# Performance work log

Hardware: AMD Instinct MI355X
Metric: run time of the kernel (lower is better)

Reference implementation:

```python
import jax, jax.numpy as jnp
import numpy as np

B, T, L, H, I, W_OUT = 64, 512, 2, 512, 128, 32


def setup_inputs() -> dict:
    key = jax.random.key(0)
    ks = jax.random.split(key, 12)
    stdv = 1.0 / np.sqrt(H)
    u = lambda k, shape: jax.random.uniform(k, shape, jnp.float32, -stdv, stdv)
    return {
        "x": jax.random.normal(ks[0], (B, T, I), jnp.float32),
        "noise": jax.random.normal(ks[1], (B, T, L, H), jnp.float32) * 0.1,
        "W_ih0": u(ks[2], (H, I)),
        "W_ih1": u(ks[3], (H, H)),
        "W_hh0": u(ks[4], (H, H)),
        "W_hh1": u(ks[5], (H, H)),
        "b_ih0": u(ks[6], (H,)),
        "b_ih1": u(ks[7], (H,)),
        "b_hh0": u(ks[8], (H,)),
        "b_hh1": u(ks[9], (H,)),
        "fc_w": u(ks[10], (W_OUT, H)),
        "fc_b": u(ks[11], (W_OUT,)),
    }


def reference(x, noise, W_ih0, W_ih1, W_hh0, W_hh1, b_ih0, b_ih1, b_hh0, b_hh1, fc_w, fc_b):
    # Sequential two-layer tanh RNN; scan over time keeps hidden state resident.
    h0 = jnp.zeros((B, H), x.dtype)
    h1 = jnp.zeros((B, H), x.dtype)

    def step(carry, inp):
        h0, h1 = carry
        x_t, n_t = inp  # x_t: [B,I], n_t: [B,L,H]
        h0 = jnp.tanh(x_t @ W_ih0.T + b_ih0 + h0 @ W_hh0.T + b_hh0 + n_t[:, 0, :])
        h1 = jnp.tanh(h0 @ W_ih1.T + b_ih1 + h1 @ W_hh1.T + b_hh1 + n_t[:, 1, :])
        return (h0, h1), None

    # time-major scan inputs
    (h0, h1), _ = jax.lax.scan(step, (h0, h1), (jnp.swapaxes(x, 0, 1), jnp.swapaxes(noise, 0, 1)))
    return h1 @ fc_w.T + fc_b  # [B, wheel_len]
```

## Files before the change

kernel.cpp:

```cpp
#include <hip/hip_runtime.h>


#define T_STEPS 512
#define NBATCH  64
#define DRING   32
#define THR_LEAD 20

typedef _Float16 half2v __attribute__((ext_vector_type(2)));
typedef _Float16 f16x8  __attribute__((ext_vector_type(8)));
typedef float    f32x4  __attribute__((ext_vector_type(4)));

__device__ __forceinline__ unsigned pack2(float a, float b) {
    _Float16 fa = (_Float16)a, fb = (_Float16)b;
    unsigned short ua = __builtin_bit_cast(unsigned short, fa);
    unsigned short ub = __builtin_bit_cast(unsigned short, fb);
    return (unsigned)ua | ((unsigned)ub << 16);
}

__device__ __forceinline__ float fast_tanh(float xv) {
    float e2 = __builtin_amdgcn_exp2f(xv * 2.885390082f);
    return 1.f - 2.f * __builtin_amdgcn_rcpf(e2 + 1.f);
}

__device__ __forceinline__ f32x4 mfma16(uint4 a, uint4 b, f32x4 c) {
    return __builtin_amdgcn_mfma_f32_16x16x32_f16(
        __builtin_bit_cast(f16x8, a), __builtin_bit_cast(f16x8, b), c, 0, 0, 0);
}

__device__ __forceinline__ void bar_lgkm() {
    asm volatile("s_waitcnt lgkmcnt(0)\n\ts_barrier" ::: "memory");
}

__device__ __forceinline__ float ntload_f(const float* p) {
    return __builtin_nontemporal_load(p);
}
__device__ __forceinline__ float2 ntload_f2(const float* p) {
    float a = __builtin_nontemporal_load(p);
    float b = __builtin_nontemporal_load(p + 1);
    return make_float2(a, b);
}

__device__ __forceinline__ unsigned poll1(unsigned long long* p, unsigned tag,
                                          long& budget) {
    unsigned long long v = __hip_atomic_load(p, __ATOMIC_RELAXED, __HIP_MEMORY_SCOPE_AGENT);
    while ((unsigned)(v >> 32) != tag && budget > 0) {
        v = __hip_atomic_load(p, __ATOMIC_RELAXED, __HIP_MEMORY_SCOPE_AGENT);
        --budget;
    }
    return (unsigned)v;
}

__device__ __forceinline__ unsigned poll_sent(unsigned long long* p,
                                              unsigned long long* sent,
                                              unsigned tag, long& budget) {
    unsigned long long sv = __hip_atomic_load(sent, __ATOMIC_RELAXED, __HIP_MEMORY_SCOPE_AGENT);
    while ((unsigned)(sv >> 32) != tag && budget > 0) {
        __builtin_amdgcn_s_sleep(1);
        sv = __hip_atomic_load(sent, __ATOMIC_RELAXED, __HIP_MEMORY_SCOPE_AGENT);
        --budget;
    }
    return poll1(p, tag, budget);
}

#define NWPF (4 * 16 * 16 * 64)

__global__ void init_pack(const float* __restrict__ Wih0, const float* __restrict__ Whh0,
                          const float* __restrict__ Wih1, const float* __restrict__ Whh1,
                          uint4* __restrict__ wp0, uint4* __restrict__ wp1,
                          int* __restrict__ prog) {
    int gid = blockIdx.x * 256 + threadIdx.x;
    if (gid == 32) prog[32] = prog[32] + 1;
    if (gid < 32) prog[gid] = 0;
    if (gid < NWPF) {
        int lane = gid & 63, f = (gid >> 6) & 15, w = (gid >> 10) & 15, s = gid >> 14;
        uint4 o = make_uint4(0, 0, 0, 0);
        if (w < 10) {
            int rt = f >> 1, ktl = f & 1;
            int r = s * 128 + rt * 16 + (lane & 15);
            unsigned dv[4];
#pragma unroll
            for (int d = 0; d < 4; ++d) {
                int kp = 32 * w + ktl * 16 + ((lane >> 4) * 4) + d;
                float w0, w1;
                if (kp < 64) { w0 = Wih0[r * 128 + 2 * kp]; w1 = Wih0[r * 128 + 2 * kp + 1]; }
                else { int p0 = kp - 64;
                       w0 = Whh0[r * 512 + 2 * p0]; w1 = Whh0[r * 512 + 2 * p0 + 1]; }
                dv[d] = pack2(w0, w1);
            }
            o = make_uint4(dv[0], dv[1], dv[2], dv[3]);
        }
        wp0[gid] = o;
    } else if (gid < 2 * NWPF) {
        int idx = gid - NWPF;
        int lane = idx & 63, f = (idx >> 6) & 15, w = (idx >> 10) & 15, s = idx >> 14;
        int rt = f >> 1, ktl = f & 1;
        int r = s * 128 + rt * 16 + (lane & 15);
        unsigned dv[4];
#pragma unroll
        for (int d = 0; d < 4; ++d) {
            int kp = 32 * w + ktl * 16 + ((lane >> 4) * 4) + d;
            float w0, w1;
            if (kp < 256) { w0 = Wih1[r * 512 + 2 * kp]; w1 = Wih1[r * 512 + 2 * kp + 1]; }
            else { int p1 = kp - 256;
                   w0 = Whh1[r * 512 + 2 * p1]; w1 = Whh1[r * 512 + 2 * p1 + 1]; }
            dv[d] = pack2(w0, w1);
        }
        wp1[idx] = make_uint4(dv[0], dv[1], dv[2], dv[3]);
    }
}

template <int LAYER>
__device__ __forceinline__ void run_layer(
    int b0, int s, int L, int pair,
    const float* __restrict__ x, const float* __restrict__ noise,
    const uint4* __restrict__ wp,
    const float* __restrict__ bih, const float* __restrict__ bhh,
    unsigned long long* __restrict__ hb0, unsigned long long* __restrict__ hb1,
    int* __restrict__ prog,
    const float* __restrict__ fcw, const float* __restrict__ fcb,
    float* __restrict__ out) {
    constexpr int NP = (LAYER == 0) ? 10 : 16;

    const int w = L >> 6, lane = L & 63;
    const int j31 = lane & 31, bbl = lane >> 5;
    const unsigned tagbase = ((unsigned)prog[32]) << 10;
    long budget = 2000000000L;

    const bool active   = (LAYER == 1) || (w < 10);
    const bool isX      = (LAYER == 0) && (w < 2);
    const bool isPF     = (LAYER == 1) && (w < 8);
    const bool isOwn    = (LAYER == 0) ? (w == 2 + 2 * s || w == 3 + 2 * s)
                                       : (w == 8 + 2 * s || w == 9 + 2 * s);
    const bool isRemote = active && !isX && !isPF && !isOwn;

    uint4 wfr[16];
#pragma unroll
    for (int f = 0; f < 16; ++f) {
        wfr[f] = wp[(size_t)(((s * 16 + w) * 16) + f) * 64 + lane];
        asm volatile("" : "+v"(wfr[f].x), "+v"(wfr[f].y), "+v"(wfr[f].z), "+v"(wfr[f].w));
    }

    __shared__ __align__(16) unsigned strip[16][64];
    __shared__ __align__(16) float psum[NP][2][128];
    for (int i = L; i < 16 * 64; i += 1024) ((unsigned*)strip)[i] = 0u;

    const bool isRed = (L < 256);
    const int bbr = L >> 7, rw = L & 127;
    const int rgl = s * 128 + rw;
    float cb = 0.f, nz = 0.f;
    if (isRed) {
        cb = bih[rgl] + bhh[rgl];
        nz = ntload_f(&noise[(((size_t)(b0 + bbr) * T_STEPS + 0) * 2 + LAYER) * 512 + rgl]);
    }
    __syncthreads();

    unsigned long long pf = 0;
    float2 xf = make_float2(0.f, 0.f);
    if constexpr (LAYER == 1) {
        if (isPF) {
            unsigned long long* base = &hb0[((size_t)0 * NBATCH + (b0 + bbl)) * 256];
            unsigned v = poll_sent(base + (32 * w + j31), base + (32 * w + 31),
                                   tagbase + 1, budget);
            pf = ((unsigned long long)(tagbase + 1) << 32) | v;
        }
    } else {
        if (isX)
            xf = ntload_f2(x + ((size_t)(b0 + bbl) * T_STEPS + 0) * 128 + 2 * (32 * w + j31));
    }

    int known = 0;
    const int colm = lane & 15, kg = lane >> 4;

    for (int t = 0; t < T_STEPS; ++t) {
        const bool last = (t == T_STEPS - 1);
        __builtin_amdgcn_s_setprio(1);

        if constexpr (LAYER == 1) {
            if (isPF) {
                unsigned want = tagbase + (unsigned)t + 1;
                if ((unsigned)(pf >> 32) != want) {
                    __builtin_amdgcn_s_setprio(0);
                    unsigned long long* base =
                        &hb0[((size_t)(t & (DRING - 1)) * NBATCH + (b0 + bbl)) * 256];
                    unsigned v = poll_sent(base + (32 * w + j31), base + (32 * w + 31),
                                           want, budget);
                    pf = ((unsigned long long)want << 32) | v;
                    __builtin_amdgcn_s_setprio(1);
                }
                strip[w][bbl * 32 + j31] = (unsigned)pf;
                if (!last)
                    pf = __hip_atomic_load(&hb0[((size_t)((t + 1) & (DRING - 1)) * NBATCH +
                                                 (b0 + bbl)) * 256 + (32 * w + j31)],
                                           __ATOMIC_RELAXED, __HIP_MEMORY_SCOPE_AGENT);
            } else if (isRemote) {
                if (t > 0) {
                    unsigned long long* base =
                        &hb1[((size_t)((t - 1) & 3) * NBATCH + (b0 + bbl)) * 256];
                    __builtin_amdgcn_s_setprio(0);
                    unsigned v = poll_sent(base + (32 * (w - 8) + j31),
                                           base + (32 * (w - 8) + 31),
                                           tagbase + (unsigned)t, budget);
                    __builtin_amdgcn_s_setprio(1);
                    strip[w][bbl * 32 + j31] = v;
                }
            }
        } else {
            if (isX) {
                strip[w][bbl * 32 + j31] = pack2(xf.x, xf.y);
                if (!last)
                    xf = ntload_f2(x + ((size_t)(b0 + bbl) * T_STEPS + (t + 1)) * 128 +
                                   2 * (32 * w + j31));
            } else if (isRemote) {
                if (t > 0) {
                    unsigned long long* base =
                        &hb0[((size_t)((t - 1) & (DRING - 1)) * NBATCH + (b0 + bbl)) * 256];
                    __builtin_amdgcn_s_setprio(0);
                    unsigned v = poll_sent(base + (32 * w - 64 + j31),
                                           base + (32 * w - 64 + 31),
                                           tagbase + (unsigned)t, budget);
                    __builtin_amdgcn_s_setprio(1);
                    strip[w][bbl * 32 + j31] = v;
                }
            }
        }

        float nznext = 0.f;
        if (!last && isRed)
            nznext = ntload_f(&noise[(((size_t)(b0 + bbr) * T_STEPS + (t + 1)) * 2 + LAYER) * 512 + rgl]);

        if (active) {
            const unsigned* sb = &strip[w][(colm & 1) * 32 + kg * 4];
            uint4 B0 = *(const uint4*)&sb[0];
            uint4 B1 = *(const uint4*)&sb[16];
#pragma unroll
            for (int rt = 0; rt < 8; ++rt) {
                f32x4 C = {0.f, 0.f, 0.f, 0.f};
                C = mfma16(wfr[2 * rt + 0], B0, C);
                C = mfma16(wfr[2 * rt + 1], B1, C);
                if (colm < 2)
                    *(f32x4*)&psum[w][colm][rt * 16 + 4 * kg] = C;
            }
        }

        bar_lgkm();

        if (isRed) {
            float sum = 0.f;
#pragma unroll
            for (int g = 0; g < NP; ++g) sum += psum[g][bbr][rw];
            float h = fast_tanh(sum + cb + nz);
            float hnb = __shfl_down(h, 1);
            if ((L & 1) == 0) {
                unsigned pv = pack2(h, hnb);
                int pr = s * 64 + (rw >> 1);
                unsigned long long atom =
                    ((unsigned long long)(tagbase + (unsigned)t + 1) << 32) |
                    (unsigned long long)pv;
                if constexpr (LAYER == 0) {
                    if (t - known > THR_LEAD) {
                        __builtin_amdgcn_s_setprio(0);
                        while (t - known > THR_LEAD && budget > 0) {
                            __builtin_amdgcn_s_sleep(2);
                            known = __hip_atomic_load(&prog[pair], __ATOMIC_RELAXED,
                                                      __HIP_MEMORY_SCOPE_AGENT);
                            --budget;
                        }
                        __builtin_amdgcn_s_setprio(1);
                    }
                    __hip_atomic_store(&hb0[((size_t)(t & (DRING - 1)) * NBATCH + (b0 + bbr)) * 256 + pr],
                                       atom, __ATOMIC_RELAXED, __HIP_MEMORY_SCOPE_AGENT);
                    strip[2 + (pr >> 5)][bbr * 32 + (pr & 31)] = pv;
                } else {
                    __hip_atomic_store(&hb1[((size_t)(t & 3) * NBATCH + (b0 + bbr)) * 256 + pr],
                                       atom, __ATOMIC_RELAXED, __HIP_MEMORY_SCOPE_AGENT);
                    strip[8 + (pr >> 5)][bbr * 32 + (pr & 31)] = pv;
                }
            }
            nz = nznext;
        }
        if constexpr (LAYER == 1) {
            if (s == 0 && L == 960 && t > 1)
                __hip_atomic_store(&prog[pair], t - 2, __ATOMIC_RELAXED,
                                   __HIP_MEMORY_SCOPE_AGENT);
        }
        bar_lgkm();
        __builtin_amdgcn_s_setprio(0);
    }

    if constexpr (LAYER == 1) {
        if (s == 0) {
            __shared__ float hs[2][512];
            __shared__ float part[2][512];
            if (L < 512) {
                int bl = L >> 8, pr = L & 255;
                unsigned v = poll1(&hb1[((size_t)((T_STEPS - 1) & 3) * NBATCH + (b0 + bl)) * 256 + pr],
                                   tagbase + (unsigned)T_STEPS, budget);
                half2v h2 = __builtin_bit_cast(half2v, v);
                hs[bl][2 * pr] = (float)h2.x; hs[bl][2 * pr + 1] = (float)h2.y;
            }
            __syncthreads();
            {
                int bl = L >> 9, rest = L & 511, o = rest & 31, seg = rest >> 5;
                const float* wr = fcw + o * 512 + seg * 32;
                const float* hr = &hs[bl][seg * 32];
                float a = 0.f;
#pragma unroll
                for (int k = 0; k < 32; ++k) a = fmaf(wr[k], hr[k], a);
                part[bl][rest] = a;
            }
            __syncthreads();
            if (L < 64) {
                int bl = L >> 5, o = L & 31;
                float ssum = fcb[o];
#pragma unroll
                for (int sgi = 0; sgi < 16; ++sgi) ssum += part[bl][sgi * 32 + o];
                out[(b0 + bl) * 32 + o] = ssum;
            }
        }
    }
}

__global__ __launch_bounds__(1024, 4)
void rnn_dual(const float* __restrict__ x, const float* __restrict__ noise,
              const uint4* __restrict__ wp0, const uint4* __restrict__ wp1,
              const float* __restrict__ bih0, const float* __restrict__ bhh0,
              const float* __restrict__ bih1, const float* __restrict__ bhh1,
              const float* __restrict__ fcw, const float* __restrict__ fcb,
              unsigned long long* __restrict__ hb0,
              unsigned long long* __restrict__ hb1,
              int* __restrict__ prog,
              float* __restrict__ out) {
    const int L = threadIdx.x;
    const int gid = blockIdx.x;
    const int cl = gid & 63;
    const int s = gid >> 6;
    const int layer = cl >> 5;
    const int pair = cl & 31;
    const int b0 = pair * 2;
    if (layer == 0)
        run_layer<0>(b0, s, L, pair, x, noise, wp0, bih0, bhh0,
                     hb0, hb1, prog, nullptr, nullptr, nullptr);
    else
        run_layer<1>(b0, s, L, pair, x, noise, wp1, bih1, bhh1,
                     hb0, hb1, prog, fcw, fcb, out);
}

extern "C" void kernel_launch(void* const* d_in, const int* in_sizes, int n_in,
                              void* d_out, int out_size, void* d_ws, size_t ws_size,
                              hipStream_t stream) {
    const float* x     = (const float*)d_in[0];
    const float* noise = (const float*)d_in[1];
    const float* Wih0  = (const float*)d_in[2];
    const float* Wih1  = (const float*)d_in[3];
    const float* Whh0  = (const float*)d_in[4];
    const float* Whh1  = (const float*)d_in[5];
    const float* bih0  = (const float*)d_in[6];
    const float* bih1  = (const float*)d_in[7];
    const float* bhh0  = (const float*)d_in[8];
    const float* bhh1  = (const float*)d_in[9];
    const float* fcw   = (const float*)d_in[10];
    const float* fcb   = (const float*)d_in[11];
    float* out = (float*)d_out;

    char* ws = (char*)d_ws;
    size_t o = 0;
    uint4* wp0 = (uint4*)(ws + o); o += (size_t)NWPF * 16;
    uint4* wp1 = (uint4*)(ws + o); o += (size_t)NWPF * 16;
    unsigned long long* hb0 = (unsigned long long*)(ws + o);
    o += (size_t)DRING * NBATCH * 256 * 8;
    unsigned long long* hb1 = (unsigned long long*)(ws + o);
    o += (size_t)4 * NBATCH * 256 * 8;
    int* prog = (int*)(ws + o); o += 33 * sizeof(int);

    const int total = 2 * NWPF;
    init_pack<<<(total + 255) / 256, 256, 0, stream>>>(Wih0, Whh0, Wih1, Whh1,
                                                       wp0, wp1, prog);
    rnn_dual<<<256, 1024, 0, stream>>>(x, noise, wp0, wp1, bih0, bhh0, bih1, bhh1,
                                       fcw, fcb, hb0, hb1, prog, out);
}
```

Baseline: 1.075 ms.

## Double-buffer partial sums, drop end-of-step barrier, poll own slice via global

Result: slower. 1.155 ms (+7.5%).

```diff
diff --git a/kernel.cpp b/kernel.cpp
--- a/kernel.cpp
+++ b/kernel.cpp
@@ -50,15 +50,18 @@
     return (unsigned)v;
 }
 
-__device__ __forceinline__ unsigned poll_sent(unsigned long long* p,
+__device__ __forceinline__ unsigned poll_spec(unsigned long long* p,
                                               unsigned long long* sent,
                                               unsigned tag, long& budget) {
+    unsigned long long v  = __hip_atomic_load(p,    __ATOMIC_RELAXED, __HIP_MEMORY_SCOPE_AGENT);
     unsigned long long sv = __hip_atomic_load(sent, __ATOMIC_RELAXED, __HIP_MEMORY_SCOPE_AGENT);
     while ((unsigned)(sv >> 32) != tag && budget > 0) {
         __builtin_amdgcn_s_sleep(1);
+        v  = __hip_atomic_load(p,    __ATOMIC_RELAXED, __HIP_MEMORY_SCOPE_AGENT);
         sv = __hip_atomic_load(sent, __ATOMIC_RELAXED, __HIP_MEMORY_SCOPE_AGENT);
         --budget;
     }
+    if ((unsigned)(v >> 32) == tag) return (unsigned)v;
     return poll1(p, tag, budget);
 }
 
@@ -126,12 +129,10 @@
     const unsigned tagbase = ((unsigned)prog[32]) << 10;
     long budget = 2000000000L;
 
-    const bool active   = (LAYER == 1) || (w < 10);
-    const bool isX      = (LAYER == 0) && (w < 2);
-    const bool isPF     = (LAYER == 1) && (w < 8);
-    const bool isOwn    = (LAYER == 0) ? (w == 2 + 2 * s || w == 3 + 2 * s)
-                                       : (w == 8 + 2 * s || w == 9 + 2 * s);
-    const bool isRemote = active && !isX && !isPF && !isOwn;
+    const bool active = (LAYER == 1) || (w < 10);
+    const bool isX    = (LAYER == 0) && (w < 2);
+    const bool isPF   = (LAYER == 1) && (w < 8);
+    const bool isPoll = (LAYER == 0) ? (w >= 2 && w < 10) : (w >= 8);
 
     uint4 wfr[16];
 #pragma unroll
@@ -141,11 +142,12 @@
     }
 
     __shared__ __align__(16) unsigned strip[16][64];
-    __shared__ __align__(16) float psum[NP][2][128];
+    __shared__ __align__(16) float psum[2][NP][2][128];
     for (int i = L; i < 16 * 64; i += 1024) ((unsigned*)strip)[i] = 0u;
 
-    const bool isRed = (L < 256);
-    const int bbr = L >> 7, rw = L & 127;
+    const bool isRed = (LAYER == 0) ? (L >= 640 && L < 896) : (L < 256);
+    const int ur  = (LAYER == 0) ? (L - 640) : L;
+    const int bbr = (ur >> 7) & 1, rw = ur & 127;
     const int rgl = s * 128 + rw;
     float cb = 0.f, nz = 0.f;
     if (isRed) {
@@ -158,9 +160,8 @@
     float2 xf = make_float2(0.f, 0.f);
     if constexpr (LAYER == 1) {
         if (isPF) {
-            unsigned long long* base = &hb0[((size_t)0 * NBATCH + (b0 + bbl)) * 256];
-            unsigned v = poll_sent(base + (32 * w + j31), base + (32 * w + 31),
-                                   tagbase + 1, budget);
+            unsigned long long* sb = &hb0[((size_t)0 * NBATCH + (b0 + bbl)) * 256 + 32 * w];
+            unsigned v = poll_spec(sb + j31, sb + 31, tagbase + 1, budget);
             pf = ((unsigned long long)(tagbase + 1) << 32) | v;
         }
     } else {
@@ -172,6 +173,7 @@
     const int colm = lane & 15, kg = lane >> 4;
 
     for (int t = 0; t < T_STEPS; ++t) {
+        const int p = t & 1;
         const bool last = (t == T_STEPS - 1);
         __builtin_amdgcn_s_setprio(1);
 
@@ -180,10 +182,9 @@
                 unsigned want = tagbase + (unsigned)t + 1;
                 if ((unsigned)(pf >> 32) != want) {
                     __builtin_amdgcn_s_setprio(0);
-                    unsigned long long* base =
-                        &hb0[((size_t)(t & (DRING - 1)) * NBATCH + (b0 + bbl)) * 256];
-                    unsigned v = poll_sent(base + (32 * w + j31), base + (32 * w + 31),
-                                           want, budget);
+                    unsigned long long* sb =
+                        &hb0[((size_t)(t & (DRING - 1)) * NBATCH + (b0 + bbl)) * 256 + 32 * w];
+                    unsigned v = poll_spec(sb + j31, sb + 31, want, budget);
                     pf = ((unsigned long long)want << 32) | v;
                     __builtin_amdgcn_s_setprio(1);
                 }
@@ -192,14 +193,12 @@
                     pf = __hip_atomic_load(&hb0[((size_t)((t + 1) & (DRING - 1)) * NBATCH +
                                                  (b0 + bbl)) * 256 + (32 * w + j31)],
                                            __ATOMIC_RELAXED, __HIP_MEMORY_SCOPE_AGENT);
-            } else if (isRemote) {
+            } else {
                 if (t > 0) {
-                    unsigned long long* base =
-                        &hb1[((size_t)((t - 1) & 3) * NBATCH + (b0 + bbl)) * 256];
+                    unsigned long long* sb =
+                        &hb1[((size_t)((t - 1) & 3) * NBATCH + (b0 + bbl)) * 256 + 32 * (w - 8)];
                     __builtin_amdgcn_s_setprio(0);
-                    unsigned v = poll_sent(base + (32 * (w - 8) + j31),
-                                           base + (32 * (w - 8) + 31),
-                                           tagbase + (unsigned)t, budget);
+                    unsigned v = poll_spec(sb + j31, sb + 31, tagbase + (unsigned)t, budget);
                     __builtin_amdgcn_s_setprio(1);
                     strip[w][bbl * 32 + j31] = v;
                 }
@@ -210,14 +209,13 @@
                 if (!last)
                     xf = ntload_f2(x + ((size_t)(b0 + bbl) * T_STEPS + (t + 1)) * 128 +
                                    2 * (32 * w + j31));
-            } else if (isRemote) {
+            } else if (isPoll) {
                 if (t > 0) {
-                    unsigned long long* base =
-                        &hb0[((size_t)((t - 1) & (DRING - 1)) * NBATCH + (b0 + bbl)) * 256];
+                    unsigned long long* sb =
+                        &hb0[((size_t)((t - 1) & (DRING - 1)) * NBATCH + (b0 + bbl)) * 256 +
+                             (32 * w - 64)];
                     __builtin_amdgcn_s_setprio(0);
-                    unsigned v = poll_sent(base + (32 * w - 64 + j31),
-                                           base + (32 * w - 64 + 31),
-                                           tagbase + (unsigned)t, budget);
+                    unsigned v = poll_spec(sb + j31, sb + 31, tagbase + (unsigned)t, budget);
                     __builtin_amdgcn_s_setprio(1);
                     strip[w][bbl * 32 + j31] = v;
                 }
@@ -238,7 +236,7 @@
                 C = mfma16(wfr[2 * rt + 0], B0, C);
                 C = mfma16(wfr[2 * rt + 1], B1, C);
                 if (colm < 2)
-                    *(f32x4*)&psum[w][colm][rt * 16 + 4 * kg] = C;
+                    *(f32x4*)&psum[p][w][colm][rt * 16 + 4 * kg] = C;
             }
         }
 
@@ -247,10 +245,10 @@
         if (isRed) {
             float sum = 0.f;
 #pragma unroll
-            for (int g = 0; g < NP; ++g) sum += psum[g][bbr][rw];
+            for (int g = 0; g < NP; ++g) sum += psum[p][g][bbr][rw];
             float h = fast_tanh(sum + cb + nz);
             float hnb = __shfl_down(h, 1);
-            if ((L & 1) == 0) {
+            if ((ur & 1) == 0) {
                 unsigned pv = pack2(h, hnb);
                 int pr = s * 64 + (rw >> 1);
                 unsigned long long atom =
@@ -269,11 +267,9 @@
                     }
                     __hip_atomic_store(&hb0[((size_t)(t & (DRING - 1)) * NBATCH + (b0 + bbr)) * 256 + pr],
                                        atom, __ATOMIC_RELAXED, __HIP_MEMORY_SCOPE_AGENT);
-                    strip[2 + (pr >> 5)][bbr * 32 + (pr & 31)] = pv;
                 } else {
                     __hip_atomic_store(&hb1[((size_t)(t & 3) * NBATCH + (b0 + bbr)) * 256 + pr],
                                        atom, __ATOMIC_RELAXED, __HIP_MEMORY_SCOPE_AGENT);
-                    strip[8 + (pr >> 5)][bbr * 32 + (pr & 31)] = pv;
                 }
             }
             nz = nznext;
@@ -283,37 +279,38 @@
                 __hip_atomic_store(&prog[pair], t - 2, __ATOMIC_RELAXED,
                                    __HIP_MEMORY_SCOPE_AGENT);
         }
-        bar_lgkm();
         __builtin_amdgcn_s_setprio(0);
     }
 
     if constexpr (LAYER == 1) {
         if (s == 0) {
-            __shared__ float hs[2][512];
-            __shared__ float part[2][512];
+            __syncthreads();
+            float* hsbuf = (float*)&psum[0][0][0][0];
+            float* partb = hsbuf + 1024;
             if (L < 512) {
                 int bl = L >> 8, pr = L & 255;
                 unsigned v = poll1(&hb1[((size_t)((T_STEPS - 1) & 3) * NBATCH + (b0 + bl)) * 256 + pr],
                                    tagbase + (unsigned)T_STEPS, budget);
                 half2v h2 = __builtin_bit_cast(half2v, v);
-                hs[bl][2 * pr] = (float)h2.x; hs[bl][2 * pr + 1] = (float)h2.y;
+                hsbuf[bl * 512 + 2 * pr] = (float)h2.x;
+                hsbuf[bl * 512 + 2 * pr + 1] = (float)h2.y;
             }
             __syncthreads();
             {
                 int bl = L >> 9, rest = L & 511, o = rest & 31, seg = rest >> 5;
                 const float* wr = fcw + o * 512 + seg * 32;
-                const float* hr = &hs[bl][seg * 32];
+                const float* hr = &hsbuf[bl * 512 + seg * 32];
                 float a = 0.f;
 #pragma unroll
                 for (int k = 0; k < 32; ++k) a = fmaf(wr[k], hr[k], a);
-                part[bl][rest] = a;
+                partb[bl * 512 + rest] = a;
             }
             __syncthreads();
             if (L < 64) {
                 int bl = L >> 5, o = L & 31;
                 float ssum = fcb[o];
 #pragma unroll
-                for (int sgi = 0; sgi < 16; ++sgi) ssum += part[bl][sgi * 32 + o];
+                for (int sgi = 0; sgi < 16; ++sgi) ssum += partb[bl * 512 + sgi * 32 + o];
                 out[(b0 + bl) * 32 + o] = ssum;
             }
         }
```
